# Kernel optimization log

Hardware: AMD Instinct MI355X
Metric: run time of the kernel (lower is better)

Reference implementation:

```python
import jax, jax.numpy as jnp
import numpy as np

B, S, H = 32, 4096, 512

def setup_inputs() -> dict:
    key = jax.random.key(0)
    k1, k2, k3, k4, k5 = jax.random.split(key, 5)
    scale = 1.0 / np.sqrt(H)
    return {
        "query": jax.random.normal(k1, (B, 1, H), dtype=jnp.float32),
        "keys": jax.random.normal(k2, (B, S, H), dtype=jnp.float32),
        "Wa": jax.random.normal(k3, (H, H), dtype=jnp.float32) * scale,
        "Ua": jax.random.normal(k4, (H, H), dtype=jnp.float32) * scale,
        "Va": jax.random.normal(k5, (H, 1), dtype=jnp.float32) * scale,
    }

def reference(query, keys, Wa, Ua, Va):
    # additive (Bahdanau) attention scores: Va^T tanh(Wa q + Ua k)
    q_proj = jnp.einsum('bqh,hd->bqd', query, Wa)          # [B,1,H]
    k_proj = jnp.einsum('bsh,hd->bsd', keys, Ua)           # [B,S,H]
    scores = jnp.einsum('bsd,d->bs', jnp.tanh(q_proj + k_proj), Va[:, 0])  # [B,S]
    weights = jax.nn.softmax(scores, axis=-1)[:, None, :]  # [B,1,S]
    context = jnp.einsum('bqs,bsh->bqh', weights, keys)    # [B,1,H]
    return (context, weights)
```

## Files before the change

kernel.cpp:

```cpp
#include <hip/hip_runtime.h>
#include <hip/hip_bf16.h>

#define B_ 32
#define S_ 4096
#define H_ 512

typedef short bf16x8 __attribute__((ext_vector_type(8)));
typedef unsigned short u16x8 __attribute__((ext_vector_type(8)));
typedef float f32x4 __attribute__((ext_vector_type(4)));

__device__ inline unsigned short f2bf(float x) {
    unsigned u = __float_as_uint(x);
    return (unsigned short)((u + 0x7fffu + ((u >> 16) & 1u)) >> 16);
}

__device__ inline float fast_tanh(float x) {
    float e = __expf(2.f * x);
    return 1.f - 2.f / (e + 1.f);
}

__device__ __forceinline__ void stage16(const void* g, void* lds_base, int lane) {
#if defined(__has_builtin) && __has_builtin(__builtin_amdgcn_global_load_lds)
    __builtin_amdgcn_global_load_lds(
        (const __attribute__((address_space(1))) unsigned char*)g,
        (__attribute__((address_space(3))) unsigned char*)lds_base, 16, 0, 0);
#else
    ((uint4*)lds_base)[lane] = *(const uint4*)g;
#endif
}

__global__ void k_prep_ua(const float* __restrict__ Ua,
                          unsigned short* __restrict__ ua_t) {
    __shared__ float tile[32][33];
    int h0 = blockIdx.x * 32, d0 = blockIdx.y * 32;
    int tx = threadIdx.x, ty = threadIdx.y;
#pragma unroll
    for (int j = 0; j < 4; ++j)
        tile[ty + j * 8][tx] = Ua[(size_t)(h0 + ty + j * 8) * H_ + d0 + tx];
    __syncthreads();
#pragma unroll
    for (int j = 0; j < 4; ++j) {
        int dl = ty + j * 8;
        ua_t[(size_t)(d0 + dl) * H_ + h0 + tx] = f2bf(tile[tx][dl]);
    }
}

__global__ __launch_bounds__(512) void k_qproj(const float* __restrict__ query,
                                               const float* __restrict__ Wa,
                                               float* __restrict__ qproj) {
    __shared__ float q[H_];
    int b = blockIdx.x, d = threadIdx.x;
    q[d] = query[(size_t)b * H_ + d];
    __syncthreads();
    float acc = 0.f;
    for (int h = 0; h < H_; ++h)
        acc = fmaf(q[h], Wa[(size_t)h * H_ + d], acc);
    qproj[(size_t)b * H_ + d] = acc;
}

__global__ __launch_bounds__(512, 4) void k_scores(
    const float* __restrict__ keys, const unsigned short* __restrict__ ua_t,
    const float* __restrict__ qproj, const float* __restrict__ Va,
    float* __restrict__ part_sc) {
    __shared__ __align__(16) unsigned char As[16384];
    __shared__ __align__(16) unsigned char Bs[16384];
    __shared__ float smp[4][128];

    int tid = threadIdx.x;
    int wave = tid >> 6, lane = tid & 63;
    int lq = lane & 15, lh = lane >> 4;
    int wm = wave >> 2;
    int wnn = wave & 3;
    int b = blockIdx.z, nb = blockIdx.y, m0 = blockIdx.x * 128;

    const float* keysb = keys + (size_t)b * S_ * H_;

    int r = tid >> 2, qtr = tid & 3;
    const float* aptr = keysb + (size_t)(m0 + r) * H_ + qtr * 16;
    unsigned aswz = (unsigned)((r & 7) << 4);
    unsigned abase = (unsigned)(r * 128);

    int rb0 = wave * 8 + (lane >> 3);
    int rb1 = 64 + rb0;
    unsigned cb = (unsigned)((lane & 7) * 16);
    const unsigned char* uab = (const unsigned char*)ua_t;
    const unsigned char* bsrc0 = uab + ((size_t)(nb * 128 + rb0)) * 1024 + (cb ^ ((rb0 & 7) << 4));
    const unsigned char* bsrc1 = uab + ((size_t)(nb * 128 + rb1)) * 1024 + (cb ^ ((rb1 & 7) << 4));
    unsigned char* ldsB0 = Bs + wave * 1024;
    unsigned char* ldsB1 = Bs + 8192 + wave * 1024;

    f32x4 acc[4][2];
#pragma unroll
    for (int i = 0; i < 4; ++i)
#pragma unroll
        for (int j = 0; j < 2; ++j) acc[i][j] = (f32x4){0.f, 0.f, 0.f, 0.f};

    unsigned swzR = (unsigned)((lq & 7) << 4);

    float4 ar[2][4];
#pragma unroll
    for (int j = 0; j < 4; ++j) ar[0][j] = *(const float4*)(aptr + j * 4);

#pragma unroll
    for (int t = 0; t < 8; ++t) {
        const int cur = t & 1, nxt = cur ^ 1;
        __syncthreads();
        if (t < 7) {
#pragma unroll
            for (int j = 0; j < 4; ++j)
                ar[nxt][j] = *(const float4*)(aptr + (t + 1) * 64 + j * 4);
        }
        stage16(bsrc0 + t * 128, ldsB0, lane);
        stage16(bsrc1 + t * 128, ldsB1, lane);
#pragma unroll
        for (int j16 = 0; j16 < 2; ++j16) {
            float4 x = ar[cur][2 * j16], y = ar[cur][2 * j16 + 1];
            u16x8 v;
            v[0] = f2bf(x.x); v[1] = f2bf(x.y); v[2] = f2bf(x.z); v[3] = f2bf(x.w);
            v[4] = f2bf(y.x); v[5] = f2bf(y.y); v[6] = f2bf(y.z); v[7] = f2bf(y.w);
            *(u16x8*)(As + abase + ((unsigned)(qtr * 32 + j16 * 16) ^ aswz)) = v;
        }
        __syncthreads();

#pragma unroll
        for (int ks = 0; ks < 2; ++ks) {
            bf16x8 af[4], bv[2];
            unsigned koff = (unsigned)(ks * 64 + lh * 16) ^ swzR;
#pragma unroll
            for (int mf = 0; mf < 4; ++mf)
                af[mf] = *(const bf16x8*)(As + (unsigned)((wm * 64 + mf * 16 + lq) * 128) + koff);
#pragma unroll
            for (int nf = 0; nf < 2; ++nf)
                bv[nf] = *(const bf16x8*)(Bs + (unsigned)((wnn * 32 + nf * 16 + lq) * 128) + koff);
#pragma unroll
            for (int mf = 0; mf < 4; ++mf)
#pragma unroll
                for (int nf = 0; nf < 2; ++nf)
                    acc[mf][nf] = __builtin_amdgcn_mfma_f32_16x16x32_bf16(
                        af[mf], bv[nf], acc[mf][nf], 0, 0, 0);
        }
    }

    float va_r[2], qp_r[2];
#pragma unroll
    for (int nf = 0; nf < 2; ++nf) {
        int n = nb * 128 + wnn * 32 + nf * 16 + lq;
        va_r[nf] = Va[n];
        qp_r[nf] = qproj[(size_t)b * H_ + n];
    }
#pragma unroll
    for (int mf = 0; mf < 4; ++mf) {
#pragma unroll
        for (int reg = 0; reg < 4; ++reg) {
            float p = va_r[0] * fast_tanh(qp_r[0] + acc[mf][0][reg])
                    + va_r[1] * fast_tanh(qp_r[1] + acc[mf][1][reg]);
            p += __shfl_xor(p, 1);
            p += __shfl_xor(p, 2);
            p += __shfl_xor(p, 4);
            p += __shfl_xor(p, 8);
            if (lq == 0) smp[wnn][wm * 64 + mf * 16 + lh * 4 + reg] = p;
        }
    }
    __syncthreads();
    if (tid < 128) {
        float s = smp[0][tid] + smp[1][tid] + smp[2][tid] + smp[3][tid];
        part_sc[((size_t)nb * B_ + b) * S_ + m0 + tid] = s;
    }
}

__global__ __launch_bounds__(512) void k_softmax(const float* __restrict__ part_sc,
                                                 float* __restrict__ wts) {
    __shared__ float red[8];
    int b = blockIdx.x, tid = threadIdx.x;
    const float* p0 = part_sc + (size_t)b * S_;
    const float* p1 = p0 + (size_t)B_ * S_;
    const float* p2 = p1 + (size_t)B_ * S_;
    const float* p3 = p2 + (size_t)B_ * S_;
    float v[8];
    float m = -1e30f;
#pragma unroll
    for (int i = 0; i < 8; ++i) {
        int s = tid + i * 512;
        v[i] = ((p0[s] + p1[s]) + (p2[s] + p3[s]));
        m = fmaxf(m, v[i]);
    }
#pragma unroll
    for (int o = 1; o < 64; o <<= 1) m = fmaxf(m, __shfl_xor(m, o));
    if ((tid & 63) == 0) red[tid >> 6] = m;
    __syncthreads();
    m = red[0];
#pragma unroll
    for (int w = 1; w < 8; ++w) m = fmaxf(m, red[w]);
    float sum = 0.f;
#pragma unroll
    for (int i = 0; i < 8; ++i) {
        v[i] = __expf(v[i] - m);
        sum += v[i];
    }
#pragma unroll
    for (int o = 1; o < 64; o <<= 1) sum += __shfl_xor(sum, o);
    __syncthreads();
    if ((tid & 63) == 0) red[tid >> 6] = sum;
    __syncthreads();
    float tot = 0.f;
#pragma unroll
    for (int w = 0; w < 8; ++w) tot += red[w];
    float inv = 1.f / tot;
#pragma unroll
    for (int i = 0; i < 8; ++i) wts[(size_t)b * S_ + tid + i * 512] = v[i] * inv;
}

__global__ __launch_bounds__(512) void k_ctx_part(const float* __restrict__ keys,
                                                  const float* __restrict__ wts,
                                                  float* __restrict__ part) {
    int c = blockIdx.x, b = blockIdx.y, h = threadIdx.x;
    const float* wrow = wts + (size_t)b * S_ + c * 128;
    const float* kbase = keys + ((size_t)b * S_ + c * 128) * H_ + h;
    float acc = 0.f;
#pragma unroll 8
    for (int s = 0; s < 128; ++s)
        acc = fmaf(wrow[s], kbase[(size_t)s * H_], acc);
    part[((size_t)c * B_ + b) * H_ + h] = acc;
}

__global__ __launch_bounds__(512) void k_ctx_reduce(const float* __restrict__ part,
                                                    float* __restrict__ ctx) {
    int b = blockIdx.x, h = threadIdx.x;
    float s = 0.f;
#pragma unroll
    for (int c = 0; c < 32; ++c) s += part[((size_t)c * B_ + b) * H_ + h];
    ctx[(size_t)b * H_ + h] = s;
}

extern "C" void kernel_launch(void* const* d_in, const int* in_sizes, int n_in,
                              void* d_out, int out_size, void* d_ws, size_t ws_size,
                              hipStream_t stream) {
    const float* query = (const float*)d_in[0];
    const float* keys  = (const float*)d_in[1];
    const float* Wa    = (const float*)d_in[2];
    const float* Ua    = (const float*)d_in[3];
    const float* Va    = (const float*)d_in[4];

    float* out = (float*)d_out;
    float* ctx = out;
    float* wts = out + B_ * H_;

    char* ws = (char*)d_ws;
    unsigned short* ua_t = (unsigned short*)ws;
    float* qproj   = (float*)(ws + 524288);
    float* part_sc = (float*)(ws + 524288 + 65536);
    float* part_cx = (float*)(ws + 524288 + 65536 + 2097152);

    k_prep_ua<<<dim3(16, 16), dim3(32, 8), 0, stream>>>(Ua, ua_t);
    k_qproj<<<dim3(32), dim3(512), 0, stream>>>(query, Wa, qproj);
    k_scores<<<dim3(32, 4, 32), dim3(512), 0, stream>>>(keys, ua_t, qproj, Va, part_sc);
    k_softmax<<<dim3(32), dim3(512), 0, stream>>>(part_sc, wts);
    k_ctx_part<<<dim3(32, 32), dim3(512), 0, stream>>>(keys, wts, part_cx);
    k_ctx_reduce<<<dim3(32), dim3(512), 0, stream>>>(part_cx, ctx);
}
```

Before: 218.8 us.

## Double-buffer LDS tiles in scores kernel and remap blocks for XCD locality

New measurement: 215.9 us. No clear change (-1.4%).

```diff
diff --git a/kernel.cpp b/kernel.cpp
--- a/kernel.cpp
+++ b/kernel.cpp
@@ -19,14 +19,10 @@
     return 1.f - 2.f / (e + 1.f);
 }
 
-__device__ __forceinline__ void stage16(const void* g, void* lds_base, int lane) {
-#if defined(__has_builtin) && __has_builtin(__builtin_amdgcn_global_load_lds)
+__device__ __forceinline__ void stage16(const void* g, void* lds_base) {
     __builtin_amdgcn_global_load_lds(
         (const __attribute__((address_space(1))) unsigned char*)g,
         (__attribute__((address_space(3))) unsigned char*)lds_base, 16, 0, 0);
-#else
-    ((uint4*)lds_base)[lane] = *(const uint4*)g;
-#endif
 }
 
 __global__ void k_prep_ua(const float* __restrict__ Ua,
@@ -58,12 +54,12 @@
     qproj[(size_t)b * H_ + d] = acc;
 }
 
-__global__ __launch_bounds__(512, 4) void k_scores(
+__global__ __launch_bounds__(512, 2) void k_scores(
     const float* __restrict__ keys, const unsigned short* __restrict__ ua_t,
     const float* __restrict__ qproj, const float* __restrict__ Va,
     float* __restrict__ part_sc) {
-    __shared__ __align__(16) unsigned char As[16384];
-    __shared__ __align__(16) unsigned char Bs[16384];
+    __shared__ __align__(16) unsigned char As[2][16384];
+    __shared__ __align__(16) unsigned char Bs[2][16384];
     __shared__ float smp[4][128];
 
     int tid = threadIdx.x;
@@ -71,13 +67,17 @@
     int lq = lane & 15, lh = lane >> 4;
     int wm = wave >> 2;
     int wnn = wave & 3;
-    int b = blockIdx.z, nb = blockIdx.y, m0 = blockIdx.x * 128;
+
+    int logical = (blockIdx.x & 7) * 512 + (blockIdx.x >> 3);
+    int b  = logical >> 7;
+    int m0 = ((logical >> 2) & 31) * 128;
+    int nb = logical & 3;
 
     const float* keysb = keys + (size_t)b * S_ * H_;
 
     int r = tid >> 2, qtr = tid & 3;
     const float* aptr = keysb + (size_t)(m0 + r) * H_ + qtr * 16;
-    unsigned aswz = (unsigned)((r & 7) << 4);
+    unsigned aswz  = (unsigned)((r & 7) << 4);
     unsigned abase = (unsigned)(r * 128);
 
     int rb0 = wave * 8 + (lane >> 3);
@@ -86,8 +86,6 @@
     const unsigned char* uab = (const unsigned char*)ua_t;
     const unsigned char* bsrc0 = uab + ((size_t)(nb * 128 + rb0)) * 1024 + (cb ^ ((rb0 & 7) << 4));
     const unsigned char* bsrc1 = uab + ((size_t)(nb * 128 + rb1)) * 1024 + (cb ^ ((rb1 & 7) << 4));
-    unsigned char* ldsB0 = Bs + wave * 1024;
-    unsigned char* ldsB1 = Bs + 8192 + wave * 1024;
 
     f32x4 acc[4][2];
 #pragma unroll
@@ -97,30 +95,33 @@
 
     unsigned swzR = (unsigned)((lq & 7) << 4);
 
-    float4 ar[2][4];
-#pragma unroll
-    for (int j = 0; j < 4; ++j) ar[0][j] = *(const float4*)(aptr + j * 4);
+    float4 arg[4];
+
+    stage16(bsrc0, &Bs[0][wave * 1024]);
+    stage16(bsrc1, &Bs[0][8192 + wave * 1024]);
+#pragma unroll
+    for (int j = 0; j < 4; ++j) arg[j] = *(const float4*)(aptr + j * 4);
+#pragma unroll
+    for (int j16 = 0; j16 < 2; ++j16) {
+        float4 x = arg[2 * j16], y = arg[2 * j16 + 1];
+        u16x8 v;
+        v[0] = f2bf(x.x); v[1] = f2bf(x.y); v[2] = f2bf(x.z); v[3] = f2bf(x.w);
+        v[4] = f2bf(y.x); v[5] = f2bf(y.y); v[6] = f2bf(y.z); v[7] = f2bf(y.w);
+        *(u16x8*)(&As[0][0] + abase + ((unsigned)(qtr * 32 + j16 * 16) ^ aswz)) = v;
+    }
+    __syncthreads();
 
 #pragma unroll
     for (int t = 0; t < 8; ++t) {
         const int cur = t & 1, nxt = cur ^ 1;
-        __syncthreads();
+
         if (t < 7) {
+            stage16(bsrc0 + (t + 1) * 128, &Bs[nxt][wave * 1024]);
+            stage16(bsrc1 + (t + 1) * 128, &Bs[nxt][8192 + wave * 1024]);
 #pragma unroll
             for (int j = 0; j < 4; ++j)
-                ar[nxt][j] = *(const float4*)(aptr + (t + 1) * 64 + j * 4);
-        }
-        stage16(bsrc0 + t * 128, ldsB0, lane);
-        stage16(bsrc1 + t * 128, ldsB1, lane);
-#pragma unroll
-        for (int j16 = 0; j16 < 2; ++j16) {
-            float4 x = ar[cur][2 * j16], y = ar[cur][2 * j16 + 1];
-            u16x8 v;
-            v[0] = f2bf(x.x); v[1] = f2bf(x.y); v[2] = f2bf(x.z); v[3] = f2bf(x.w);
-            v[4] = f2bf(y.x); v[5] = f2bf(y.y); v[6] = f2bf(y.z); v[7] = f2bf(y.w);
-            *(u16x8*)(As + abase + ((unsigned)(qtr * 32 + j16 * 16) ^ aswz)) = v;
-        }
-        __syncthreads();
+                arg[j] = *(const float4*)(aptr + (t + 1) * 64 + j * 4);
+        }
 
 #pragma unroll
         for (int ks = 0; ks < 2; ++ks) {
@@ -128,10 +129,10 @@
             unsigned koff = (unsigned)(ks * 64 + lh * 16) ^ swzR;
 #pragma unroll
             for (int mf = 0; mf < 4; ++mf)
-                af[mf] = *(const bf16x8*)(As + (unsigned)((wm * 64 + mf * 16 + lq) * 128) + koff);
+                af[mf] = *(const bf16x8*)(&As[cur][0] + (unsigned)((wm * 64 + mf * 16 + lq) * 128) + koff);
 #pragma unroll
             for (int nf = 0; nf < 2; ++nf)
-                bv[nf] = *(const bf16x8*)(Bs + (unsigned)((wnn * 32 + nf * 16 + lq) * 128) + koff);
+                bv[nf] = *(const bf16x8*)(&Bs[cur][0] + (unsigned)((wnn * 32 + nf * 16 + lq) * 128) + koff);
 #pragma unroll
             for (int mf = 0; mf < 4; ++mf)
 #pragma unroll
@@ -139,6 +140,19 @@
                     acc[mf][nf] = __builtin_amdgcn_mfma_f32_16x16x32_bf16(
                         af[mf], bv[nf], acc[mf][nf], 0, 0, 0);
         }
+
+        if (t < 7) {
+#pragma unroll
+            for (int j16 = 0; j16 < 2; ++j16) {
+                float4 x = arg[2 * j16], y = arg[2 * j16 + 1];
+                u16x8 v;
+                v[0] = f2bf(x.x); v[1] = f2bf(x.y); v[2] = f2bf(x.z); v[3] = f2bf(x.w);
+                v[4] = f2bf(y.x); v[5] = f2bf(y.y); v[6] = f2bf(y.z); v[7] = f2bf(y.w);
+                *(u16x8*)(&As[nxt][0] + abase + ((unsigned)(qtr * 32 + j16 * 16) ^ aswz)) = v;
+            }
+        }
+
+        __syncthreads();
     }
 
     float va_r[2], qp_r[2];
@@ -253,7 +267,7 @@
 
     k_prep_ua<<<dim3(16, 16), dim3(32, 8), 0, stream>>>(Ua, ua_t);
     k_qproj<<<dim3(32), dim3(512), 0, stream>>>(query, Wa, qproj);
-    k_scores<<<dim3(32, 4, 32), dim3(512), 0, stream>>>(keys, ua_t, qproj, Va, part_sc);
+    k_scores<<<dim3(4096), dim3(512), 0, stream>>>(keys, ua_t, qproj, Va, part_sc);
     k_softmax<<<dim3(32), dim3(512), 0, stream>>>(part_sc, wts);
     k_ctx_part<<<dim3(32, 32), dim3(512), 0, stream>>>(keys, wts, part_cx);
     k_ctx_reduce<<<dim3(32), dim3(512), 0, stream>>>(part_cx, ctx);
```
